# Kernel optimization log

Measured on AMD Instinct MI355X. Metric: run time of the kernel, lower is better.

## Reference

```python
import jax, jax.numpy as jnp
import numpy as np
from math import sqrt

N = 4096      # points
I = 64        # in_channels
H = 64        # hidden_units
O = 64        # out_channels
CUTS = 8
GROUPS = 4
RADIUS = 1.0
BLK = 128     # i-block size for the pairwise interaction (KeOps-style tiling)
EPS = 1e-5


def leaky(x):
    return jnp.where(x >= 0, x, 0.2 * x)


def group_norm(x, w, b):
    # x: (N, C). Matches torch GroupNorm on input (1, C, N):
    # stats per group over (C//GROUPS, N) jointly, affine per channel.
    n, c = x.shape
    xg = x.reshape(n, GROUPS, c // GROUPS)
    mean = xg.mean(axis=(0, 2), keepdims=True)
    var = ((xg - mean) ** 2).mean(axis=(0, 2), keepdims=True)
    xn = ((xg - mean) * jax.lax.rsqrt(var + EPS)).reshape(n, c)
    return xn * w + b


def setup_inputs() -> dict:
    key = jax.random.key(0)
    ks = jax.random.split(key, 16)
    rn = lambda k, s, sc=1.0: jax.random.normal(k, s, jnp.float32) * sc
    # conv MLP init as in the torch module
    A1 = rn(ks[3], (CUTS, 3))                                   # nn.init.normal_
    c1 = jax.random.uniform(ks[4], (CUTS,)) * 0.8 * jnp.sqrt((A1 ** 2).sum(-1))
    A2 = jax.random.uniform(ks[5], (H, CUTS), minval=-1.0 / np.sqrt(CUTS), maxval=1.0 / np.sqrt(CUTS))
    c2 = rn(ks[6], (H,)) * 0.5 * jnp.sqrt((A2 ** 2).sum(-1))
    return {
        "points": rn(ks[0], (N, 3)),
        "nuv": rn(ks[1], (N, 3, 3)),
        "features": rn(ks[2], (N, I)),
        "W_in1": rn(ks[7], (H, I), 1.0 / np.sqrt(I)), "b_in1": jnp.zeros((H,)),
        "W_in2": rn(ks[8], (H, H), 1.0 / np.sqrt(H)), "b_in2": jnp.zeros((H,)),
        "gn_in_w": jnp.ones((H,)), "gn_in_b": jnp.zeros((H,)),
        "A1": A1, "c1": c1, "A2": A2, "c2": c2,
        "W_out1": rn(ks[9], (O, H), 1.0 / np.sqrt(H)), "b_out1": jnp.zeros((O,)),
        "W_out2": rn(ks[10], (O, O), 1.0 / np.sqrt(O)), "b_out2": jnp.zeros((O,)),
        "gn_out_w": jnp.ones((O,)), "gn_out_b": jnp.zeros((O,)),
    }


def reference(points, nuv, features, W_in1, b_in1, W_in2, b_in2, gn_in_w, gn_in_b,
              A1, c1, A2, c2, W_out1, b_out1, W_out2, b_out2, gn_out_w, gn_out_b):
    # 1. net_in MLP + GroupNorm over (1, H, N)
    f = leaky(leaky(features @ W_in1.T + b_in1) @ W_in2.T + b_in2)
    f = group_norm(f, gn_in_w, gn_in_b)                      # (N, H)

    pts = points / (sqrt(2.0) * RADIUS)                      # scaled coords
    n_j = jax.lax.stop_gradient(nuv[:, 0, :])                # j-side normals are detached

    # 2. pairwise quasi-geodesic interaction, tiled over i-blocks.
    # Per-head loop in the original just slices rows of A2/c2 and channels of f;
    # computing the full H-dim conv and reducing is the identical math.
    @jax.checkpoint
    def block(args):
        xi, nuvi = args                                      # (BLK,3), (BLK,3,3)
        diff = pts[None, :, :] - xi[:, None, :]              # (BLK, N, 3) = x_j - x_i
        dot = nuvi[:, 0, :] @ n_j.T                          # (BLK, N) <n_i, n_j>
        d2 = (diff ** 2).sum(-1) * (2.0 - dot) ** 2          # quasi-geodesic d^2
        w = jnp.exp(-d2)                                     # gaussian window w_ij
        X = jnp.einsum('bij,bnj->bni', nuvi, diff)           # P_ij in local basis (BLK,N,3)
        h = jax.nn.relu(jnp.einsum('bni,ci->bnc', X, A1) + c1)   # (BLK,N,CUTS)
        Xc = jax.nn.relu(jnp.einsum('bnc,hc->bnh', h, A2) + c2)  # (BLK,N,H)
        return jnp.einsum('bn,bnh,nh->bh', w, Xc, f)         # sum over j -> (BLK,H)

    out = jax.lax.map(block, (pts.reshape(-1, BLK, 3), nuv.reshape(-1, BLK, 3, 3)))
    out = out.reshape(N, H)

    # 3. net_out MLP + GroupNorm
    g = leaky(leaky(out @ W_out1.T + b_out1) @ W_out2.T + b_out2)
    return group_norm(g, gn_out_w, gn_out_b)                 # (N, O)
```

## Files before the change

kernel.cpp:

```cpp
#include <hip/hip_runtime.h>
#include <hip/hip_bf16.h>
#include <math.h>

#define N_PTS 4096
#define INV_SQRT2 0.70710678118654752440f

typedef float f32x4 __attribute__((ext_vector_type(4)));
typedef short s16x4 __attribute__((ext_vector_type(4)));
typedef short s16x8 __attribute__((ext_vector_type(8)));
typedef _Float16 f16x2 __attribute__((ext_vector_type(2)));

__device__ inline short f2bf(float x) {
    __hip_bfloat16 h = __float2bfloat16(x);
    return __builtin_bit_cast(short, h);
}

__device__ inline unsigned pk_trunc(float hi, float lo) {
    return __builtin_amdgcn_perm(__builtin_bit_cast(unsigned, hi),
                                 __builtin_bit_cast(unsigned, lo),
                                 0x07060302u);
}
__device__ inline unsigned pk_relu(unsigned x) {
    f16x2 v = __builtin_bit_cast(f16x2, x);
    f16x2 z = {(_Float16)0.f, (_Float16)0.f};
    return __builtin_bit_cast(unsigned, __builtin_elementwise_max(v, z));
}
__device__ inline float rfl(float x) {
    return __builtin_bit_cast(float, __builtin_amdgcn_readfirstlane(__builtin_bit_cast(int, x)));
}

#if defined(__has_builtin)
#  if __has_builtin(__builtin_amdgcn_mfma_f32_16x16x16bf16_1k)
#    define MFMA16(a, b, c) __builtin_amdgcn_mfma_f32_16x16x16bf16_1k((a), (b), (c), 0, 0, 0)
#    define HAVE_MFMA16 1
#  elif __has_builtin(__builtin_amdgcn_mfma_f32_16x16x16_bf16)
#    define MFMA16(a, b, c) __builtin_amdgcn_mfma_f32_16x16x16_bf16((a), (b), (c), 0, 0, 0)
#    define HAVE_MFMA16 1
#  endif
#endif
#ifndef HAVE_MFMA16
__device__ inline f32x4 mfma16_asm(s16x4 a, s16x4 b, f32x4 c) {
    asm volatile("s_nop 1\n\tv_mfma_f32_16x16x16_bf16 %0, %1, %2, %0"
                 : "+v"(c) : "v"(a), "v"(b));
    return c;
}
#  define MFMA16(a, b, c) mfma16_asm((a), (b), (c))
#endif

#if defined(__has_builtin) && __has_builtin(__builtin_amdgcn_global_load_lds)
#  define HAVE_GLDS 1
#endif

__global__ __launch_bounds__(256) void mlp_gn_kernel(
    const float* __restrict__ inp, int extra,
    const float* __restrict__ W1, const float* __restrict__ b1,
    const float* __restrict__ W2, const float* __restrict__ b2,
    float* __restrict__ pre_out, float* __restrict__ partials)
{
    __shared__ float in_s[4][64];
    __shared__ float h1_s[4][64];
    __shared__ float red_s[4][8];

    const int tid = threadIdx.x;
    const int lane = tid & 63;
    const int wid = tid >> 6;
    const int n0 = blockIdx.x * 4;

    float xin = inp[n0 * 64 + tid];
    for (int s = 1; s <= extra; ++s)
        xin += inp[(size_t)s * (N_PTS * 64) + n0 * 64 + tid];
    in_s[wid][lane] = xin;
    __syncthreads();

    const int c = lane;
    float h = b1[c];
#pragma unroll
    for (int k4 = 0; k4 < 16; ++k4) {
        float4 wv = *(const float4*)&W1[c * 64 + k4 * 4];
        h = fmaf(in_s[wid][k4*4+0], wv.x, h);
        h = fmaf(in_s[wid][k4*4+1], wv.y, h);
        h = fmaf(in_s[wid][k4*4+2], wv.z, h);
        h = fmaf(in_s[wid][k4*4+3], wv.w, h);
    }
    h = (h >= 0.f) ? h : 0.2f * h;
    h1_s[wid][c] = h;
    __syncthreads();

    float g = b2[c];
#pragma unroll
    for (int k4 = 0; k4 < 16; ++k4) {
        float4 wv = *(const float4*)&W2[c * 64 + k4 * 4];
        g = fmaf(h1_s[wid][k4*4+0], wv.x, g);
        g = fmaf(h1_s[wid][k4*4+1], wv.y, g);
        g = fmaf(h1_s[wid][k4*4+2], wv.z, g);
        g = fmaf(h1_s[wid][k4*4+3], wv.w, g);
    }
    g = (g >= 0.f) ? g : 0.2f * g;
    pre_out[n0 * 64 + tid] = g;

    float v = g, v2 = g * g;
#pragma unroll
    for (int m = 1; m < 16; m <<= 1) {
        v  += __shfl_xor(v,  m, 64);
        v2 += __shfl_xor(v2, m, 64);
    }
    if ((lane & 15) == 0) {
        int grp = lane >> 4;
        red_s[wid][grp * 2 + 0] = v;
        red_s[wid][grp * 2 + 1] = v2;
    }
    __syncthreads();
    if (tid < 8) {
        int grp = tid >> 1, which = tid & 1;
        float s = red_s[0][grp*2+which] + red_s[1][grp*2+which]
                + red_s[2][grp*2+which] + red_s[3][grp*2+which];
        partials[blockIdx.x * 8 + grp * 2 + which] = s;
    }
}

__global__ __launch_bounds__(256) void finalize_kernel(
    const float* __restrict__ partials, int nblocks,
    const float* __restrict__ gw, const float* __restrict__ gb,
    float* __restrict__ ss)
{
    __shared__ float red[8][32];
    __shared__ float mean_s[4], inv_s[4];
    const int t = threadIdx.x;
    const int s = t >> 5, slot = t & 31;
    float acc = 0.f;
    for (int b = slot; b < nblocks; b += 32) acc += partials[b * 8 + s];
    red[s][slot] = acc;
    __syncthreads();
    if (t < 8) {
        float v = 0.f;
#pragma unroll
        for (int k = 0; k < 32; ++k) v += red[t][k];
        red[t][0] = v;
    }
    __syncthreads();
    if (t < 4) {
        float S = red[t * 2][0], SS = red[t * 2 + 1][0];
        const float cnt = (float)N_PTS * 16.f;
        float mean = S / cnt;
        float var = SS / cnt - mean * mean;
        mean_s[t] = mean;
        inv_s[t] = rsqrtf(var + 1e-5f);
    }
    __syncthreads();
    if (t < 64) {
        int grp = t >> 4;
        float sc = gw[t] * inv_s[grp];
        ss[t] = sc;
        ss[64 + t] = gb[t] - mean_s[grp] * sc;
    }
}

__global__ __launch_bounds__(256) void fnt_kernel(
    const float* __restrict__ f_pre, const float* __restrict__ ss,
    short* __restrict__ fn_sw,
    const float* __restrict__ points, const float* __restrict__ nuv,
    float* __restrict__ ptn4)
{
    const int h = blockIdx.x >> 4;
    const int j = ((blockIdx.x & 15) << 8) + threadIdx.x;
    float v = f_pre[j * 64 + h] * ss[h] + ss[64 + h];
    const int t = j >> 6, jj = j & 63;
    const int jsub = jj >> 4, g = (jj >> 2) & 3, r = jj & 3;
    const int u = g * 4 + jsub, p = u >> 1, lo = u & 1;
    const int pp = p ^ (h & 7);
    fn_sw[t * 4096 + h * 64 + pp * 8 + lo * 4 + r] = f2bf(v);

    if (blockIdx.x < 16) {
        const int pt = blockIdx.x * 256 + threadIdx.x;
        float sx = points[pt*3+0] * INV_SQRT2;
        float sy = points[pt*3+1] * INV_SQRT2;
        float sz = points[pt*3+2] * INV_SQRT2;
        float nx = nuv[pt*9+0], ny = nuv[pt*9+1], nz = nuv[pt*9+2];
        *(float4*)&ptn4[pt*8 + 0] = (float4){sx, sy, sz, 0.f};
        *(float4*)&ptn4[pt*8 + 4] = (float4){nx, ny, nz, 0.f};
    }
}

__global__ __launch_bounds__(256, 4) void pairwise_kernel(
    const float* __restrict__ nuv,
    const float* __restrict__ ptn4,
    const short* __restrict__ fn_sw,
    const float* __restrict__ A1, const float* __restrict__ c1,
    const float* __restrict__ A2, const float* __restrict__ c2,
    float* __restrict__ out_part, int nt, int jshift)
{
    __shared__ __align__(16) short FS[2][4096];
    __shared__ __align__(16) short P_s[8][64*12 + 16];

    const int tid = threadIdx.x;
    const int l = tid & 63;
    const int wid = tid >> 6;
    const int g = l >> 4;
    const int hl = l & 15;

    const int js = blockIdx.x & ((1 << jshift) - 1);
    const int ig = blockIdx.x >> jshift;
    const int i0 = ig * 8 + wid * 2;
    const int jbase = js * nt * 64;
    const int tmask = nt - 1;

    float s_nv[2][9], s_pi[2][3];
#pragma unroll
    for (int ii = 0; ii < 2; ++ii) {
#pragma unroll
        for (int k = 0; k < 9; ++k) s_nv[ii][k] = rfl(nuv[(i0 + ii) * 9 + k]);
#pragma unroll
        for (int k = 0; k < 3; ++k) s_pi[ii][k] = rfl(ptn4[(i0 + ii) * 8 + k]);
    }
    float a1v[8][3], c1v[8];
#pragma unroll
    for (int cc = 0; cc < 8; ++cc) {
        a1v[cc][0] = A1[cc*3+0]; a1v[cc][1] = A1[cc*3+1]; a1v[cc][2] = A1[cc*3+2];
        c1v[cc] = c1[cc];
    }

    s16x4 A2sB[4];
#pragma unroll
    for (int ht = 0; ht < 4; ++ht) {
        const int h = ht * 16 + hl;
        s16x4 v;
#pragma unroll
        for (int r = 0; r < 4; ++r) {
            const int cc = 4 * g + r;
            float val = (cc < 8) ? A2[h*8 + cc] : ((cc == 8) ? c2[h] : 0.f);
            v[r] = f2bf(val);
        }
        A2sB[ht] = v;
    }

    f32x4 acc0[4], acc1[4];
#pragma unroll
    for (int ht = 0; ht < 4; ++ht) {
        acc0[ht] = (f32x4){0.f, 0.f, 0.f, 0.f};
        acc1[ht] = (f32x4){0.f, 0.f, 0.f, 0.f};
    }

    const char* FSb = (const char*)&FS[0][0];
    const int fs_off0 = hl * 128 + ((((g << 1) | 0) ^ (hl & 7)) << 4);
    const int fs_off1 = hl * 128 + ((((g << 1) | 1) ^ (hl & 7)) << 4);

    auto stage = [&](int buf, int t) {
        const short* src = fn_sw + (size_t)(js * nt + t) * 4096;
#ifdef HAVE_GLDS
        const short* s0 = src + wid * 1024 + l * 8;
        short* d0 = &FS[buf][wid * 1024];
        __builtin_amdgcn_global_load_lds((const unsigned int*)s0,
                                         (unsigned int*)d0, 16, 0, 0);
        __builtin_amdgcn_global_load_lds((const unsigned int*)(s0 + 512),
                                         (unsigned int*)(d0 + 512), 16, 0, 0);
#else
        s16x8 a = *(const s16x8*)(src + tid * 16);
        s16x8 b = *(const s16x8*)(src + tid * 16 + 8);
        *(s16x8*)&FS[buf][tid * 16] = a;
        *(s16x8*)&FS[buf][tid * 16 + 8] = b;
#endif
    };

    const float* pbase = ptn4 + (size_t)jbase * 8;
    float4 pj_c = *(const float4*)&pbase[l * 8];
    float4 nj_c = *(const float4*)&pbase[l * 8 + 4];
    stage(0, 0);

    auto tile = [&](const int t, const int cur) {
        __syncthreads();
        if (t < nt - 1) stage(cur ^ 1, t + 1);

        const int tn = (t + 1) & tmask;
        float4 pj_n = *(const float4*)&pbase[(tn * 64 + l) * 8];
        float4 nj_n = *(const float4*)&pbase[(tn * 64 + l) * 8 + 4];

#pragma unroll
        for (int ii = 0; ii < 2; ++ii) {
            float dx = pj_c.x - s_pi[ii][0];
            float dy = pj_c.y - s_pi[ii][1];
            float dz = pj_c.z - s_pi[ii][2];
            float s1 = dx*dx + dy*dy + dz*dz;
            float dot = s_nv[ii][0]*nj_c.x + s_nv[ii][1]*nj_c.y + s_nv[ii][2]*nj_c.z;
            float t2v = 2.f - dot;
            float d2 = s1 * t2v * t2v;
            float w = __expf(-d2);
            float X0 = s_nv[ii][0]*dx + s_nv[ii][1]*dy + s_nv[ii][2]*dz;
            float X1 = s_nv[ii][3]*dx + s_nv[ii][4]*dy + s_nv[ii][5]*dz;
            float X2 = s_nv[ii][6]*dx + s_nv[ii][7]*dy + s_nv[ii][8]*dz;

            float hv[8];
#pragma unroll
            for (int cc = 0; cc < 8; ++cc) {
                float tt = fmaf(X0, a1v[cc][0],
                           fmaf(X1, a1v[cc][1],
                           fmaf(X2, a1v[cc][2], c1v[cc])));
                hv[cc] = tt * w;
            }
            int2 ra, rb, rc;
            ra.x = (int)pk_relu(pk_trunc(hv[1], hv[0]));
            ra.y = (int)pk_relu(pk_trunc(hv[3], hv[2]));
            rb.x = (int)pk_relu(pk_trunc(hv[5], hv[4]));
            rb.y = (int)pk_relu(pk_trunc(hv[7], hv[6]));
            rc.x = (int)(__builtin_bit_cast(unsigned, w) >> 16);
            rc.y = 0;
            short* rp = &P_s[wid * 2 + ii][l * 12];
            *(int2*)(rp + 0) = ra;
            *(int2*)(rp + 4) = rb;
            *(int2*)(rp + 8) = rc;
        }

#pragma unroll
        for (int jp = 0; jp < 2; ++jp) {
            s16x8 F[4];
            const int fo = (jp == 0) ? fs_off0 : fs_off1;
#pragma unroll
            for (int ht = 0; ht < 4; ++ht)
                F[ht] = *(const s16x8*)(FSb + cur * 8192 + ht * 2048 + fo);
#pragma unroll
            for (int lo = 0; lo < 2; ++lo) {
                const int jsub = jp * 2 + lo;
                const s16x4 Af0 = *(const s16x4*)&P_s[wid*2+0][(jsub*16 + hl)*12 + 4*g];
                const s16x4 Af1 = *(const s16x4*)&P_s[wid*2+1][(jsub*16 + hl)*12 + 4*g];
#pragma unroll
                for (int ht = 0; ht < 4; ++ht) {
                    const s16x4 fnf = lo
                        ? __builtin_shufflevector(F[ht], F[ht], 4, 5, 6, 7)
                        : __builtin_shufflevector(F[ht], F[ht], 0, 1, 2, 3);
                    f32x4 Z0 = MFMA16(Af0, A2sB[ht], ((f32x4){0.f,0.f,0.f,0.f}));
                    int2 a0;
                    a0.x = (int)pk_relu(pk_trunc(Z0[1], Z0[0]));
                    a0.y = (int)pk_relu(pk_trunc(Z0[3], Z0[2]));
                    acc0[ht] = MFMA16(fnf, __builtin_bit_cast(s16x4, a0), acc0[ht]);
                    f32x4 Z1 = MFMA16(Af1, A2sB[ht], ((f32x4){0.f,0.f,0.f,0.f}));
                    int2 a1;
                    a1.x = (int)pk_relu(pk_trunc(Z1[1], Z1[0]));
                    a1.y = (int)pk_relu(pk_trunc(Z1[3], Z1[2]));
                    acc1[ht] = MFMA16(fnf, __builtin_bit_cast(s16x4, a1), acc1[ht]);
                }
            }
        }
        pj_c = pj_n; nj_c = nj_n;
    };

    for (int tp = 0; tp < nt; tp += 2) {
        tile(tp, 0);
        tile(tp + 1, 1);
    }

    asm volatile("s_nop 7\n\ts_nop 7" ::: );

    if (g == (hl >> 2)) {
        const int r = hl & 3;
        float* ob = out_part + (size_t)js * (N_PTS * 64);
#pragma unroll
        for (int ht = 0; ht < 4; ++ht) {
            float v0 = (r == 0) ? acc0[ht][0] : (r == 1) ? acc0[ht][1]
                     : (r == 2) ? acc0[ht][2] : acc0[ht][3];
            float v1 = (r == 0) ? acc1[ht][0] : (r == 1) ? acc1[ht][1]
                     : (r == 2) ? acc1[ht][2] : acc1[ht][3];
            ob[(i0 + 0) * 64 + ht * 16 + hl] = v0;
            ob[(i0 + 1) * 64 + ht * 16 + hl] = v1;
        }
    }
}

__global__ __launch_bounds__(256) void apply_kernel(
    const float* __restrict__ pre, const float* __restrict__ ss,
    float* __restrict__ out)
{
    int idx = blockIdx.x * 256 + threadIdx.x;
    int c = idx & 63;
    out[idx] = pre[idx] * ss[c] + ss[64 + c];
}

extern "C" void kernel_launch(void* const* d_in, const int* in_sizes, int n_in,
                              void* d_out, int out_size, void* d_ws, size_t ws_size,
                              hipStream_t stream) {
    const float* points   = (const float*)d_in[0];
    const float* nuv      = (const float*)d_in[1];
    const float* features = (const float*)d_in[2];
    const float* W_in1    = (const float*)d_in[3];
    const float* b_in1    = (const float*)d_in[4];
    const float* W_in2    = (const float*)d_in[5];
    const float* b_in2    = (const float*)d_in[6];
    const float* gn_in_w  = (const float*)d_in[7];
    const float* gn_in_b  = (const float*)d_in[8];
    const float* A1       = (const float*)d_in[9];
    const float* c1       = (const float*)d_in[10];
    const float* A2       = (const float*)d_in[11];
    const float* c2       = (const float*)d_in[12];
    const float* W_out1   = (const float*)d_in[13];
    const float* b_out1   = (const float*)d_in[14];
    const float* W_out2   = (const float*)d_in[15];
    const float* b_out2   = (const float*)d_in[16];
    const float* gn_out_w = (const float*)d_in[17];
    const float* gn_out_b = (const float*)d_in[18];

    const size_t MB = 1048576;
    const int JS = (ws_size >= 5 * MB) ? 4 : 2;
    const int jshift = (JS == 4) ? 2 : 1;
    const int nt = 64 / JS;
    const size_t op_bytes = (size_t)JS * N_PTS * 64 * 4;

    char* ws = (char*)d_ws;
    float* out_part = (float*)(ws + 0);
    float* f_pre    = (float*)(ws + 0);
    float* g_pre    = (float*)(ws + 0);
    short* fn_sw    = (short*)(ws + op_bytes);
    float* ptn4     = (float*)(ws + op_bytes + 524288);
    char*  tail     = ws + op_bytes + 524288 + 131072;
    float* part_in  = (float*)(tail);
    float* part_out = (float*)(tail + 32768);
    float* ss_in    = (float*)(tail + 65536);
    float* ss_out   = (float*)(tail + 66048);

    float* outp = (float*)d_out;

    mlp_gn_kernel<<<1024, 256, 0, stream>>>(features, 0, W_in1, b_in1,
                                            W_in2, b_in2, f_pre, part_in);
    finalize_kernel<<<1, 256, 0, stream>>>(part_in, 1024, gn_in_w, gn_in_b, ss_in);
    fnt_kernel<<<1024, 256, 0, stream>>>(f_pre, ss_in, fn_sw, points, nuv, ptn4);

    pairwise_kernel<<<512 * JS, 256, 0, stream>>>(nuv, ptn4, fn_sw,
                                                  A1, c1, A2, c2, out_part,
                                                  nt, jshift);

    mlp_gn_kernel<<<1024, 256, 0, stream>>>(out_part, JS - 1, W_out1, b_out1,
                                            W_out2, b_out2, g_pre, part_out);
    finalize_kernel<<<1, 256, 0, stream>>>(part_out, 1024, gn_out_w, gn_out_b, ss_out);

    apply_kernel<<<1024, 256, 0, stream>>>(g_pre, ss_out, outp);
}
```

Measured before the change: 174.7 us.

## Single-buffer F tile in registers and pack i-pair math into float2 FMAs

Replaces the double-buffered LDS F tile with a single buffer. Each tile's F fragments are read into registers up front, then a second barrier is taken before the next tile is staged into the same buffer. This halves the F shared memory, which may raise occupancy, but it adds a barrier per tile and holds more live registers. The per-pair geometry and first-layer MLP for the two i points are also vectorised into f32x2 FMAs so the compiler can emit packed FP32 instructions.

```diff
diff --git a/kernel.cpp b/kernel.cpp
--- a/kernel.cpp
+++ b/kernel.cpp
@@ -6,6 +6,7 @@
 #define INV_SQRT2 0.70710678118654752440f
 
 typedef float f32x4 __attribute__((ext_vector_type(4)));
+typedef float f32x2 __attribute__((ext_vector_type(2)));
 typedef short s16x4 __attribute__((ext_vector_type(4)));
 typedef short s16x8 __attribute__((ext_vector_type(8)));
 typedef _Float16 f16x2 __attribute__((ext_vector_type(2)));
@@ -27,6 +28,10 @@
 }
 __device__ inline float rfl(float x) {
     return __builtin_bit_cast(float, __builtin_amdgcn_readfirstlane(__builtin_bit_cast(int, x)));
+}
+__device__ inline f32x2 bc2(float s) { return (f32x2){s, s}; }
+__device__ inline f32x2 fma2(f32x2 a, f32x2 b, f32x2 c) {
+    return __builtin_elementwise_fma(a, b, c);
 }
 
 #if defined(__has_builtin)
@@ -189,8 +194,8 @@
     const float* __restrict__ A2, const float* __restrict__ c2,
     float* __restrict__ out_part, int nt, int jshift)
 {
-    __shared__ __align__(16) short FS[2][4096];
-    __shared__ __align__(16) short P_s[8][64*12 + 16];
+    __shared__ __align__(16) short FS[4096];
+    __shared__ __align__(16) short P_s[8][768];
 
     const int tid = threadIdx.x;
     const int l = tid & 63;
@@ -201,17 +206,16 @@
     const int js = blockIdx.x & ((1 << jshift) - 1);
     const int ig = blockIdx.x >> jshift;
     const int i0 = ig * 8 + wid * 2;
-    const int jbase = js * nt * 64;
     const int tmask = nt - 1;
 
-    float s_nv[2][9], s_pi[2][3];
-#pragma unroll
-    for (int ii = 0; ii < 2; ++ii) {
-#pragma unroll
-        for (int k = 0; k < 9; ++k) s_nv[ii][k] = rfl(nuv[(i0 + ii) * 9 + k]);
-#pragma unroll
-        for (int k = 0; k < 3; ++k) s_pi[ii][k] = rfl(ptn4[(i0 + ii) * 8 + k]);
-    }
+    f32x2 nv2[9];
+#pragma unroll
+    for (int k = 0; k < 9; ++k)
+        nv2[k] = (f32x2){rfl(nuv[i0 * 9 + k]), rfl(nuv[(i0 + 1) * 9 + k])};
+    const f32x2 pix2 = (f32x2){rfl(ptn4[i0*8+0]), rfl(ptn4[(i0+1)*8+0])};
+    const f32x2 piy2 = (f32x2){rfl(ptn4[i0*8+1]), rfl(ptn4[(i0+1)*8+1])};
+    const f32x2 piz2 = (f32x2){rfl(ptn4[i0*8+2]), rfl(ptn4[(i0+1)*8+2])};
+
     float a1v[8][3], c1v[8];
 #pragma unroll
     for (int cc = 0; cc < 8; ++cc) {
@@ -240,15 +244,15 @@
         acc1[ht] = (f32x4){0.f, 0.f, 0.f, 0.f};
     }
 
-    const char* FSb = (const char*)&FS[0][0];
+    const char* FSb = (const char*)&FS[0];
     const int fs_off0 = hl * 128 + ((((g << 1) | 0) ^ (hl & 7)) << 4);
     const int fs_off1 = hl * 128 + ((((g << 1) | 1) ^ (hl & 7)) << 4);
 
-    auto stage = [&](int buf, int t) {
+    auto stage = [&](int t) {
         const short* src = fn_sw + (size_t)(js * nt + t) * 4096;
 #ifdef HAVE_GLDS
         const short* s0 = src + wid * 1024 + l * 8;
-        short* d0 = &FS[buf][wid * 1024];
+        short* d0 = &FS[wid * 1024];
         __builtin_amdgcn_global_load_lds((const unsigned int*)s0,
                                          (unsigned int*)d0, 16, 0, 0);
         __builtin_amdgcn_global_load_lds((const unsigned int*)(s0 + 512),
@@ -256,66 +260,86 @@
 #else
         s16x8 a = *(const s16x8*)(src + tid * 16);
         s16x8 b = *(const s16x8*)(src + tid * 16 + 8);
-        *(s16x8*)&FS[buf][tid * 16] = a;
-        *(s16x8*)&FS[buf][tid * 16 + 8] = b;
+        *(s16x8*)&FS[tid * 16] = a;
+        *(s16x8*)&FS[tid * 16 + 8] = b;
 #endif
     };
 
-    const float* pbase = ptn4 + (size_t)jbase * 8;
+    const float* pbase = ptn4 + (size_t)(js * nt) * 64 * 8;
     float4 pj_c = *(const float4*)&pbase[l * 8];
     float4 nj_c = *(const float4*)&pbase[l * 8 + 4];
-    stage(0, 0);
-
-    auto tile = [&](const int t, const int cur) {
+    stage(0);
+
+    for (int t = 0; t < nt; ++t) {
         __syncthreads();
-        if (t < nt - 1) stage(cur ^ 1, t + 1);
+
+        s16x8 Fr0[4], Fr1[4];
+#pragma unroll
+        for (int ht = 0; ht < 4; ++ht) {
+            Fr0[ht] = *(const s16x8*)(FSb + ht * 2048 + fs_off0);
+            Fr1[ht] = *(const s16x8*)(FSb + ht * 2048 + fs_off1);
+        }
+        __syncthreads();
+        if (t < nt - 1) stage(t + 1);
 
         const int tn = (t + 1) & tmask;
         float4 pj_n = *(const float4*)&pbase[(tn * 64 + l) * 8];
         float4 nj_n = *(const float4*)&pbase[(tn * 64 + l) * 8 + 4];
 
-#pragma unroll
-        for (int ii = 0; ii < 2; ++ii) {
-            float dx = pj_c.x - s_pi[ii][0];
-            float dy = pj_c.y - s_pi[ii][1];
-            float dz = pj_c.z - s_pi[ii][2];
-            float s1 = dx*dx + dy*dy + dz*dz;
-            float dot = s_nv[ii][0]*nj_c.x + s_nv[ii][1]*nj_c.y + s_nv[ii][2]*nj_c.z;
-            float t2v = 2.f - dot;
-            float d2 = s1 * t2v * t2v;
-            float w = __expf(-d2);
-            float X0 = s_nv[ii][0]*dx + s_nv[ii][1]*dy + s_nv[ii][2]*dz;
-            float X1 = s_nv[ii][3]*dx + s_nv[ii][4]*dy + s_nv[ii][5]*dz;
-            float X2 = s_nv[ii][6]*dx + s_nv[ii][7]*dy + s_nv[ii][8]*dz;
-
-            float hv[8];
+        {
+            f32x2 dx = bc2(pj_c.x) - pix2;
+            f32x2 dy = bc2(pj_c.y) - piy2;
+            f32x2 dz = bc2(pj_c.z) - piz2;
+            f32x2 s1 = fma2(dz, dz, fma2(dy, dy, dx * dx));
+            f32x2 dt = fma2(nv2[2], bc2(nj_c.z),
+                       fma2(nv2[1], bc2(nj_c.y), nv2[0] * bc2(nj_c.x)));
+            f32x2 t2 = bc2(2.f) - dt;
+            f32x2 d2 = (s1 * t2) * t2;
+            float w0 = __expf(-d2[0]);
+            float w1 = __expf(-d2[1]);
+            f32x2 wp = (f32x2){w0, w1};
+            f32x2 X0 = fma2(nv2[2], dz, fma2(nv2[1], dy, nv2[0] * dx));
+            f32x2 X1 = fma2(nv2[5], dz, fma2(nv2[4], dy, nv2[3] * dx));
+            f32x2 X2 = fma2(nv2[8], dz, fma2(nv2[7], dy, nv2[6] * dx));
+
+            f32x2 hv[8];
 #pragma unroll
             for (int cc = 0; cc < 8; ++cc) {
-                float tt = fmaf(X0, a1v[cc][0],
-                           fmaf(X1, a1v[cc][1],
-                           fmaf(X2, a1v[cc][2], c1v[cc])));
-                hv[cc] = tt * w;
+                f32x2 tt = fma2(bc2(a1v[cc][2]), X2,
+                           fma2(bc2(a1v[cc][1]), X1,
+                           fma2(bc2(a1v[cc][0]), X0, bc2(c1v[cc]))));
+                hv[cc] = tt * wp;
             }
-            int2 ra, rb, rc;
-            ra.x = (int)pk_relu(pk_trunc(hv[1], hv[0]));
-            ra.y = (int)pk_relu(pk_trunc(hv[3], hv[2]));
-            rb.x = (int)pk_relu(pk_trunc(hv[5], hv[4]));
-            rb.y = (int)pk_relu(pk_trunc(hv[7], hv[6]));
-            rc.x = (int)(__builtin_bit_cast(unsigned, w) >> 16);
-            rc.y = 0;
-            short* rp = &P_s[wid * 2 + ii][l * 12];
-            *(int2*)(rp + 0) = ra;
-            *(int2*)(rp + 4) = rb;
-            *(int2*)(rp + 8) = rc;
+            {
+                int2 ra, rb, rc;
+                ra.x = (int)pk_relu(pk_trunc(hv[1][0], hv[0][0]));
+                ra.y = (int)pk_relu(pk_trunc(hv[3][0], hv[2][0]));
+                rb.x = (int)pk_relu(pk_trunc(hv[5][0], hv[4][0]));
+                rb.y = (int)pk_relu(pk_trunc(hv[7][0], hv[6][0]));
+                rc.x = (int)(__builtin_bit_cast(unsigned, w0) >> 16);
+                rc.y = 0;
+                short* rp = &P_s[wid * 2 + 0][l * 12];
+                *(int2*)(rp + 0) = ra;
+                *(int2*)(rp + 4) = rb;
+                *(int2*)(rp + 8) = rc;
+            }
+            {
+                int2 ra, rb, rc;
+                ra.x = (int)pk_relu(pk_trunc(hv[1][1], hv[0][1]));
+                ra.y = (int)pk_relu(pk_trunc(hv[3][1], hv[2][1]));
+                rb.x = (int)pk_relu(pk_trunc(hv[5][1], hv[4][1]));
+                rb.y = (int)pk_relu(pk_trunc(hv[7][1], hv[6][1]));
+                rc.x = (int)(__builtin_bit_cast(unsigned, w1) >> 16);
+                rc.y = 0;
+                short* rp = &P_s[wid * 2 + 1][l * 12];
+                *(int2*)(rp + 0) = ra;
+                *(int2*)(rp + 4) = rb;
+                *(int2*)(rp + 8) = rc;
+            }
         }
 
 #pragma unroll
         for (int jp = 0; jp < 2; ++jp) {
-            s16x8 F[4];
-            const int fo = (jp == 0) ? fs_off0 : fs_off1;
-#pragma unroll
-            for (int ht = 0; ht < 4; ++ht)
-                F[ht] = *(const s16x8*)(FSb + cur * 8192 + ht * 2048 + fo);
 #pragma unroll
             for (int lo = 0; lo < 2; ++lo) {
                 const int jsub = jp * 2 + lo;
@@ -323,9 +347,10 @@
                 const s16x4 Af1 = *(const s16x4*)&P_s[wid*2+1][(jsub*16 + hl)*12 + 4*g];
 #pragma unroll
                 for (int ht = 0; ht < 4; ++ht) {
+                    const s16x8 Fv = jp ? Fr1[ht] : Fr0[ht];
                     const s16x4 fnf = lo
-                        ? __builtin_shufflevector(F[ht], F[ht], 4, 5, 6, 7)
-                        : __builtin_shufflevector(F[ht], F[ht], 0, 1, 2, 3);
+                        ? __builtin_shufflevector(Fv, Fv, 4, 5, 6, 7)
+                        : __builtin_shufflevector(Fv, Fv, 0, 1, 2, 3);
                     f32x4 Z0 = MFMA16(Af0, A2sB[ht], ((f32x4){0.f,0.f,0.f,0.f}));
                     int2 a0;
                     a0.x = (int)pk_relu(pk_trunc(Z0[1], Z0[0]));
@@ -340,11 +365,6 @@
             }
         }
         pj_c = pj_n; nj_c = nj_n;
-    };
-
-    for (int tp = 0; tp < nt; tp += 2) {
-        tile(tp, 0);
-        tile(tp + 1, 1);
     }
 
     asm volatile("s_nop 7\n\ts_nop 7" ::: );
```

Measured after the change: 175.2 us. Within noise of the previous version (+0.3%).
